# Kernel optimization log

Measured on AMD Instinct MI355X. Metric: run time of the kernel, lower is better.

The kernel has to match this reference:

```python
import jax, jax.numpy as jnp
import numpy as np

T_SCALE = 10.0   # self.t = ones(1)*10
EPS = 1e-8       # torch cosine_similarity eps


def setup_inputs() -> dict:
    key = jax.random.key(0)
    k1, k2, k3 = jax.random.split(key, 3)
    B, D, C = 2048, 25088, 100
    feature = jax.random.normal(k1, (B, D), dtype=jnp.float32)
    label = jax.random.randint(k2, (B,), 0, C, dtype=jnp.int64)
    # mimic reset_parameters: uniform(-stdv, stdv), stdv = 1/sqrt(in_dim)
    stdv = 1.0 / np.sqrt(D)
    weight = jax.random.uniform(k3, (C, D), dtype=jnp.float32, minval=-stdv, maxval=stdv)
    return {"feature": feature, "label": label, "weight": weight}


def _cos_logits(feature, weight):
    # Equivalent to t * cosine_similarity over broadcasted (B, C, D):
    # L2-normalize rows (with torch's eps clamp on norms) then matmul.
    fn = feature / jnp.maximum(jnp.linalg.norm(feature, axis=-1, keepdims=True), EPS)
    wn = weight / jnp.maximum(jnp.linalg.norm(weight, axis=-1, keepdims=True), EPS)
    return T_SCALE * jnp.einsum('bd,cd->bc', fn, wn)  # [B, C]


def reference(feature, label, weight):
    pred = _cos_logits(feature, weight)                      # [B, C]
    logp = jax.nn.log_softmax(pred, axis=-1)
    valid = (label >= 0)
    safe_label = jnp.where(valid, label, 0)
    nll = -jnp.take_along_axis(logp, safe_label[:, None], axis=1)[:, 0]
    vmask = valid.astype(pred.dtype)
    n_valid = jnp.sum(vmask)
    loss = jnp.sum(nll * vmask) / jnp.maximum(n_valid, 1.0)  # CE with ignore_index=-1
    preds = jnp.argmax(pred, axis=1)
    acc = jnp.sum(vmask * (preds == label).astype(pred.dtype)) / (n_valid + 1e-10)
    return loss, acc
```

## Files before the change

### kernel.cpp

```cpp
#include <hip/hip_runtime.h>
#include <hip/hip_bf16.h>

#define D_DIM   25088
#define B_ROWS  2048
#define C_CLS   100
#define NT      7
#define NPAD    112
#define KSTEPS_TOTAL 784
#define SPLITS  56
#define KSTEPS_PER (KSTEPS_TOTAL / SPLITS)
#define EPS     1e-8f

typedef __bf16 bf16x8 __attribute__((ext_vector_type(8)));
typedef float  f32x4  __attribute__((ext_vector_type(4)));
typedef float  f32x2  __attribute__((ext_vector_type(2)));

__device__ __forceinline__ unsigned bfpack2(float lo, float hi) {
    unsigned a = __builtin_bit_cast(unsigned, lo);
    unsigned b = __builtin_bit_cast(unsigned, hi);
    a += 0x7FFFu + ((a >> 16) & 1u);
    b += 0x7FFFu + ((b >> 16) & 1u);
    return (a >> 16) | (b & 0xFFFF0000u);
}

__global__ __launch_bounds__(256) void prep_kernel(const float* __restrict__ w,
                                                   float* __restrict__ wscale,
                                                   unsigned* __restrict__ wpack) {
    int c = blockIdx.x;
    int t = c >> 4, n = c & 15;
    bool real = (c < C_CLS);
    const float* row = w + (size_t)c * D_DIM;
    float s = 0.f;
    for (int i = 0; i < 49; ++i) {
        int d = i * 512 + threadIdx.x * 2;
        f32x2 v = {0.f, 0.f};
        if (real) v = *(const f32x2*)(row + d);
        s += v[0]*v[0] + v[1]*v[1];
        int gstep = d >> 5, r = d & 31, quad = r >> 3, j = r & 7;
        unsigned dw = bfpack2(v[0], v[1]);
        size_t idx = ((size_t)(gstep * 7 + t) * 64 + quad * 16 + n) * 4 + (j >> 1);
        wpack[idx] = dw;
    }
    if (!real) return;
    __shared__ float red[4];
    for (int o = 32; o; o >>= 1) s += __shfl_down(s, o, 64);
    if ((threadIdx.x & 63) == 0) red[threadIdx.x >> 6] = s;
    __syncthreads();
    if (threadIdx.x == 0) {
        float nn = sqrtf(red[0] + red[1] + red[2] + red[3]);
        wscale[c] = 1.0f / fmaxf(nn, EPS);
    }
}

__global__ __launch_bounds__(256, 4) void gemm_kernel(const float* __restrict__ feat,
                                                      const uint4* __restrict__ wpack,
                                                      float* __restrict__ pred,
                                                      float* __restrict__ fnorm2) {
    int tid  = threadIdx.x;
    int wave = tid >> 6, lane = tid & 63;
    int m = lane & 15, quad = lane >> 4;
    int rowbase = blockIdx.x * 64 + wave * 16;
    int row = rowbase + m;
    int gstep0 = blockIdx.y * KSTEPS_PER;

    const float* pA = feat + (size_t)row * D_DIM + gstep0 * 32 + quad * 8;
    const uint4* pB = wpack + (size_t)gstep0 * NT * 64 + lane;

    f32x4 acc[NT];
#pragma unroll
    for (int t = 0; t < NT; ++t) acc[t] = (f32x4){0.f,0.f,0.f,0.f};
    float sumsq = 0.f;

    f32x4 a0 = *(const f32x4*)(pA);
    f32x4 a1 = *(const f32x4*)(pA + 4);

    for (int s = 0; s < KSTEPS_PER; ++s) {
        const float* pn = pA + ((s + 1 < KSTEPS_PER) ? 32 : 0);
        f32x4 n0 = *(const f32x4*)(pn);
        f32x4 n1 = *(const f32x4*)(pn + 4);

        sumsq += a0[0]*a0[0] + a0[1]*a0[1] + a0[2]*a0[2] + a0[3]*a0[3]
               + a1[0]*a1[0] + a1[1]*a1[1] + a1[2]*a1[2] + a1[3]*a1[3];
        uint4 ap;
        ap.x = bfpack2(a0[0], a0[1]);
        ap.y = bfpack2(a0[2], a0[3]);
        ap.z = bfpack2(a1[0], a1[1]);
        ap.w = bfpack2(a1[2], a1[3]);
        bf16x8 afrag = __builtin_bit_cast(bf16x8, ap);
#pragma unroll
        for (int t = 0; t < NT; ++t) {
            bf16x8 bfrag = __builtin_bit_cast(bf16x8, pB[t * 64]);
            acc[t] = __builtin_amdgcn_mfma_f32_16x16x32_bf16(afrag, bfrag, acc[t], 0, 0, 0);
        }
        a0 = n0; a1 = n1;
        pA += 32;
        pB += NT * 64;
    }

    sumsq += __shfl_xor(sumsq, 16, 64);
    sumsq += __shfl_xor(sumsq, 32, 64);
    if (quad == 0) atomicAdd(&fnorm2[row], sumsq);

#pragma unroll
    for (int t = 0; t < NT; ++t) {
#pragma unroll
        for (int r = 0; r < 4; ++r) {
            int orow = rowbase + quad * 4 + r;
            int ocol = t * 16 + m;
            atomicAdd(&pred[(size_t)orow * NPAD + ocol], acc[t][r]);
        }
    }
}

__global__ __launch_bounds__(256) void finalize_kernel(const float* __restrict__ pred,
                                                       const float* __restrict__ fnorm2,
                                                       const float* __restrict__ wscale,
                                                       const int* __restrict__ label,
                                                       float* __restrict__ scal) {
    int gwave = (blockIdx.x * 256 + threadIdx.x) >> 6;
    int lane = threadIdx.x & 63;
    int row = gwave;
    if (row >= B_ROWS) return;
    float finv = 10.0f / fmaxf(sqrtf(fnorm2[row]), EPS);
    const float* pr = pred + (size_t)row * NPAD;

    int c0 = lane, c1 = lane + 64;
    float l0 = (c0 < C_CLS) ? pr[c0] * wscale[c0] * finv : -1e30f;
    float l1 = (c1 < C_CLS) ? pr[c1] * wscale[c1] * finv : -1e30f;

    float mx = l0; int am = c0;
    if (l1 > mx) { mx = l1; am = c1; }
    for (int o = 1; o < 64; o <<= 1) {
        float om = __shfl_xor(mx, o, 64);
        int   oa = __shfl_xor(am, o, 64);
        if (om > mx || (om == mx && oa < am)) { mx = om; am = oa; }
    }
    float se = expf(l0 - mx) + expf(l1 - mx);
    for (int o = 1; o < 64; o <<= 1) se += __shfl_xor(se, o, 64);

    int lab = label[row];
    int labc = (lab < 0) ? 0 : lab;
    float lv = (labc >= 64) ? l1 : l0;
    float ll = __shfl(lv, labc & 63, 64);

    if (lane == 0 && lab >= 0) {
        float lse = mx + logf(se);
        atomicAdd(&scal[0], lse - ll);
        atomicAdd(&scal[1], (am == lab) ? 1.f : 0.f);
        atomicAdd(&scal[2], 1.f);
    }
}

__global__ void out_kernel(const float* __restrict__ scal, float* __restrict__ out) {
    out[0] = scal[0] / fmaxf(scal[2], 1.0f);
    out[1] = scal[1] / (scal[2] + 1e-10f);
}

extern "C" void kernel_launch(void* const* d_in, const int* in_sizes, int n_in,
                              void* d_out, int out_size, void* d_ws, size_t ws_size,
                              hipStream_t stream) {
    const float* feat   = (const float*)d_in[0];
    const int*   label  = (const int*)d_in[1];
    const float* weight = (const float*)d_in[2];
    float* out = (float*)d_out;

    char* ws = (char*)d_ws;
    float* pred   = (float*)(ws);
    float* fnorm2 = (float*)(ws + 917504);
    float* scal   = (float*)(ws + 925696);
    float* wscale = (float*)(ws + 925712);
    uint4* wpack  = (uint4*)(ws + 926720);

    hipMemsetAsync(ws, 0, 925712, stream);
    prep_kernel<<<NPAD, 256, 0, stream>>>(weight, wscale, (unsigned*)wpack);
    gemm_kernel<<<dim3(B_ROWS / 64, SPLITS), 256, 0, stream>>>(feat, wpack, pred, fnorm2);
    finalize_kernel<<<B_ROWS / 4 / 64, 256, 0, stream>>>(pred, fnorm2, wscale, label, scal);
    out_kernel<<<1, 1, 0, stream>>>(scal, out);
}
```

Baseline: 364.7 us.

## Parallelize weight prep over K, double split-K, deepen feature prefetch, fix finalize grid

```diff
diff --git a/kernel.cpp b/kernel.cpp
--- a/kernel.cpp
+++ b/kernel.cpp
@@ -7,13 +7,13 @@
 #define NT      7
 #define NPAD    112
 #define KSTEPS_TOTAL 784
-#define SPLITS  56
+#define SPLITS  112
 #define KSTEPS_PER (KSTEPS_TOTAL / SPLITS)
+#define PREP_G  4
 #define EPS     1e-8f
 
 typedef __bf16 bf16x8 __attribute__((ext_vector_type(8)));
 typedef float  f32x4  __attribute__((ext_vector_type(4)));
-typedef float  f32x2  __attribute__((ext_vector_type(2)));
 
 __device__ __forceinline__ unsigned bfpack2(float lo, float hi) {
     unsigned a = __builtin_bit_cast(unsigned, lo);
@@ -23,39 +23,43 @@
     return (a >> 16) | (b & 0xFFFF0000u);
 }
 
-__global__ __launch_bounds__(256) void prep_kernel(const float* __restrict__ w,
-                                                   float* __restrict__ wscale,
-                                                   unsigned* __restrict__ wpack) {
-    int c = blockIdx.x;
-    int t = c >> 4, n = c & 15;
+__global__ __launch_bounds__(448) void prep_kernel(const float* __restrict__ w,
+                                                   float* __restrict__ wnorm2,
+                                                   uint4* __restrict__ wpack) {
+    int tid  = threadIdx.x;
+    int t    = tid >> 6;
+    int quad = (tid >> 4) & 3;
+    int n    = tid & 15;
+    int c    = t * 16 + n;
     bool real = (c < C_CLS);
-    const float* row = w + (size_t)c * D_DIM;
+    const float* row = w + (size_t)c * D_DIM + quad * 8;
     float s = 0.f;
-    for (int i = 0; i < 49; ++i) {
-        int d = i * 512 + threadIdx.x * 2;
-        f32x2 v = {0.f, 0.f};
-        if (real) v = *(const f32x2*)(row + d);
-        s += v[0]*v[0] + v[1]*v[1];
-        int gstep = d >> 5, r = d & 31, quad = r >> 3, j = r & 7;
-        unsigned dw = bfpack2(v[0], v[1]);
-        size_t idx = ((size_t)(gstep * 7 + t) * 64 + quad * 16 + n) * 4 + (j >> 1);
-        wpack[idx] = dw;
+#pragma unroll
+    for (int g = 0; g < PREP_G; ++g) {
+        int gstep = blockIdx.x * PREP_G + g;
+        f32x4 v0 = {0.f,0.f,0.f,0.f}, v1 = {0.f,0.f,0.f,0.f};
+        if (real) {
+            v0 = *(const f32x4*)(row + gstep * 32);
+            v1 = *(const f32x4*)(row + gstep * 32 + 4);
+        }
+        s += v0[0]*v0[0] + v0[1]*v0[1] + v0[2]*v0[2] + v0[3]*v0[3]
+           + v1[0]*v1[0] + v1[1]*v1[1] + v1[2]*v1[2] + v1[3]*v1[3];
+        uint4 o;
+        o.x = bfpack2(v0[0], v0[1]);
+        o.y = bfpack2(v0[2], v0[3]);
+        o.z = bfpack2(v1[0], v1[1]);
+        o.w = bfpack2(v1[2], v1[3]);
+        wpack[(size_t)gstep * 448 + tid] = o;
     }
-    if (!real) return;
-    __shared__ float red[4];
-    for (int o = 32; o; o >>= 1) s += __shfl_down(s, o, 64);
-    if ((threadIdx.x & 63) == 0) red[threadIdx.x >> 6] = s;
-    __syncthreads();
-    if (threadIdx.x == 0) {
-        float nn = sqrtf(red[0] + red[1] + red[2] + red[3]);
-        wscale[c] = 1.0f / fmaxf(nn, EPS);
-    }
+    s += __shfl_xor(s, 16, 64);
+    s += __shfl_xor(s, 32, 64);
+    if (quad == 0 && real) atomicAdd(&wnorm2[c], s);
 }
 
-__global__ __launch_bounds__(256, 4) void gemm_kernel(const float* __restrict__ feat,
-                                                      const uint4* __restrict__ wpack,
-                                                      float* __restrict__ pred,
-                                                      float* __restrict__ fnorm2) {
+__global__ __launch_bounds__(256) void gemm_kernel(const float* __restrict__ feat,
+                                                   const uint4* __restrict__ wpack,
+                                                   float* __restrict__ pred,
+                                                   float* __restrict__ fnorm2) {
     int tid  = threadIdx.x;
     int wave = tid >> 6, lane = tid & 63;
     int m = lane & 15, quad = lane >> 4;
@@ -71,30 +75,32 @@
     for (int t = 0; t < NT; ++t) acc[t] = (f32x4){0.f,0.f,0.f,0.f};
     float sumsq = 0.f;
 
-    f32x4 a0 = *(const f32x4*)(pA);
-    f32x4 a1 = *(const f32x4*)(pA + 4);
+    f32x4 c0 = *(const f32x4*)(pA);
+    f32x4 c1 = *(const f32x4*)(pA + 4);
+    f32x4 n0 = *(const f32x4*)(pA + 32);
+    f32x4 n1 = *(const f32x4*)(pA + 36);
 
+#pragma unroll
     for (int s = 0; s < KSTEPS_PER; ++s) {
-        const float* pn = pA + ((s + 1 < KSTEPS_PER) ? 32 : 0);
-        f32x4 n0 = *(const f32x4*)(pn);
-        f32x4 n1 = *(const f32x4*)(pn + 4);
-
-        sumsq += a0[0]*a0[0] + a0[1]*a0[1] + a0[2]*a0[2] + a0[3]*a0[3]
-               + a1[0]*a1[0] + a1[1]*a1[1] + a1[2]*a1[2] + a1[3]*a1[3];
+        f32x4 f0 = c0, f1 = c1;
+        if (s + 2 < KSTEPS_PER) {
+            f0 = *(const f32x4*)(pA + (s + 2) * 32);
+            f1 = *(const f32x4*)(pA + (s + 2) * 32 + 4);
+        }
+        sumsq += c0[0]*c0[0] + c0[1]*c0[1] + c0[2]*c0[2] + c0[3]*c0[3]
+               + c1[0]*c1[0] + c1[1]*c1[1] + c1[2]*c1[2] + c1[3]*c1[3];
         uint4 ap;
-        ap.x = bfpack2(a0[0], a0[1]);
-        ap.y = bfpack2(a0[2], a0[3]);
-        ap.z = bfpack2(a1[0], a1[1]);
-        ap.w = bfpack2(a1[2], a1[3]);
+        ap.x = bfpack2(c0[0], c0[1]);
+        ap.y = bfpack2(c0[2], c0[3]);
+        ap.z = bfpack2(c1[0], c1[1]);
+        ap.w = bfpack2(c1[2], c1[3]);
         bf16x8 afrag = __builtin_bit_cast(bf16x8, ap);
 #pragma unroll
         for (int t = 0; t < NT; ++t) {
-            bf16x8 bfrag = __builtin_bit_cast(bf16x8, pB[t * 64]);
+            bf16x8 bfrag = __builtin_bit_cast(bf16x8, pB[s * NT * 64 + t * 64]);
             acc[t] = __builtin_amdgcn_mfma_f32_16x16x32_bf16(afrag, bfrag, acc[t], 0, 0, 0);
         }
-        a0 = n0; a1 = n1;
-        pA += 32;
-        pB += NT * 64;
+        c0 = n0; c1 = n1; n0 = f0; n1 = f1;
     }
 
     sumsq += __shfl_xor(sumsq, 16, 64);
@@ -114,19 +120,19 @@
 
 __global__ __launch_bounds__(256) void finalize_kernel(const float* __restrict__ pred,
                                                        const float* __restrict__ fnorm2,
-                                                       const float* __restrict__ wscale,
+                                                       const float* __restrict__ wnorm2,
                                                        const int* __restrict__ label,
                                                        float* __restrict__ scal) {
-    int gwave = (blockIdx.x * 256 + threadIdx.x) >> 6;
+    int row = (blockIdx.x * 256 + threadIdx.x) >> 6;
     int lane = threadIdx.x & 63;
-    int row = gwave;
     if (row >= B_ROWS) return;
     float finv = 10.0f / fmaxf(sqrtf(fnorm2[row]), EPS);
     const float* pr = pred + (size_t)row * NPAD;
 
     int c0 = lane, c1 = lane + 64;
-    float l0 = (c0 < C_CLS) ? pr[c0] * wscale[c0] * finv : -1e30f;
-    float l1 = (c1 < C_CLS) ? pr[c1] * wscale[c1] * finv : -1e30f;
+    float l0 = -1e30f, l1 = -1e30f;
+    if (c0 < C_CLS) l0 = pr[c0] * (finv / fmaxf(sqrtf(wnorm2[c0]), EPS));
+    if (c1 < C_CLS) l1 = pr[c1] * (finv / fmaxf(sqrtf(wnorm2[c1]), EPS));
 
     float mx = l0; int am = c0;
     if (l1 > mx) { mx = l1; am = c1; }
@@ -168,12 +174,12 @@
     float* pred   = (float*)(ws);
     float* fnorm2 = (float*)(ws + 917504);
     float* scal   = (float*)(ws + 925696);
-    float* wscale = (float*)(ws + 925712);
+    float* wnorm2 = (float*)(ws + 925712);
     uint4* wpack  = (uint4*)(ws + 926720);
 
-    hipMemsetAsync(ws, 0, 925712, stream);
-    prep_kernel<<<NPAD, 256, 0, stream>>>(weight, wscale, (unsigned*)wpack);
+    hipMemsetAsync(ws, 0, 926160, stream);
+    prep_kernel<<<KSTEPS_TOTAL / PREP_G, 448, 0, stream>>>(weight, wnorm2, wpack);
     gemm_kernel<<<dim3(B_ROWS / 64, SPLITS), 256, 0, stream>>>(feat, wpack, pred, fnorm2);
-    finalize_kernel<<<B_ROWS / 4 / 64, 256, 0, stream>>>(pred, fnorm2, wscale, label, scal);
+    finalize_kernel<<<B_ROWS / 4, 256, 0, stream>>>(pred, fnorm2, wnorm2, label, scal);
     out_kernel<<<1, 1, 0, stream>>>(scal, out);
 }
```

Result: slower. 422.4 us (+15.8%).
